# Kernel optimization log

Hardware: AMD Instinct MI355X
Metric: run time of the kernel (lower is better)

## Reference

```python
import jax, jax.numpy as jnp
import numpy as np

B, NMAX, H = 1024, 100, 768
A_EMB, N_EMB, C_EMB = 128, 256, 64
NEG = -1e30


def setup_inputs() -> dict:
    key = jax.random.key(0)
    ks = jax.random.split(key, 24)
    inp = {
        "pooled": jax.random.normal(ks[0], (B, H), jnp.float32),
        "x_coord": jax.random.uniform(ks[1], (1, B), jnp.float32),
        "node1": jax.random.normal(ks[2], (B, H), jnp.float32),
        "node2": jax.random.normal(ks[3], (B, H), jnp.float32),
        "neigh1": jax.random.normal(ks[4], (B, NMAX, H), jnp.float32),
        "neigh2": jax.random.normal(ks[5], (B, NMAX, H), jnp.float32),
        "dist1": jax.random.uniform(ks[6], (B, NMAX), jnp.float32),
        "dist2": jax.random.uniform(ks[7], (B, NMAX), jnp.float32),
        "len1": jnp.maximum(jax.random.randint(ks[8], (B,), 0, NMAX + 1), 1),
        "len2": jnp.maximum(jax.random.randint(ks[9], (B,), 0, NMAX + 1), 1),
    }
    s = 0.02
    d1 = H + 2 * C_EMB + N_EMB  # 1152
    inp.update({
        "Ww": jax.random.normal(ks[10], (H, A_EMB), jnp.float32) * s,
        "bw": jnp.zeros((A_EMB,), jnp.float32),
        "Wa": jax.random.normal(ks[11], (2 * A_EMB, 1), jnp.float32) * s,
        "ba": jnp.zeros((1,), jnp.float32),
        "Wdb": jax.random.normal(ks[12], (1, 1), jnp.float32) * s,
        "bdb": jnp.zeros((1,), jnp.float32),
        "Wn": jax.random.normal(ks[13], (2 * A_EMB, N_EMB), jnp.float32) * s,
        "bn": jnp.zeros((N_EMB,), jnp.float32),
        "Wc": jax.random.normal(ks[14], (1, 2 * C_EMB), jnp.float32) * s,
        "bc": jnp.zeros((2 * C_EMB,), jnp.float32),
        "W1": jax.random.normal(ks[15], (d1, d1 // 2), jnp.float32) * s,
        "b1": jnp.zeros((d1 // 2,), jnp.float32),
        "W2": jax.random.normal(ks[16], (d1 // 2, 2), jnp.float32) * s,
        "b2": jnp.zeros((2,), jnp.float32),
    })
    return inp


def _side(node, neigh, dist, mask, Ww, bw, Wa, ba, Wdb, bdb):
    # node: [B,H], neigh: [B,N,H], dist: [B,N], mask: [B,N] bool
    wn = node @ Ww + bw                         # [B,a]
    wng = jnp.einsum('bnh,ha->bna', neigh, Ww) + bw  # [B,N,a]
    cat = jnp.concatenate([jnp.broadcast_to(wn[:, None, :], wng.shape), wng], -1)
    score = jax.nn.leaky_relu(cat @ Wa + ba, 0.01)   # [B,N,1]
    score = score + dist[..., None] * Wdb[0, 0] + bdb
    score = jnp.where(mask[..., None], score, NEG)
    att = jax.nn.softmax(score, axis=1)              # softmax over neighbors
    ctx = jnp.sum(wng * att, axis=1)                 # [B,a]
    return ctx * wn


def reference(pooled, x_coord, node1, node2, neigh1, neigh2, dist1, dist2,
              len1, len2, Ww, bw, Wa, ba, Wdb, bdb, Wn, bn, Wc, bc, W1, b1, W2, b2):
    ar = jnp.arange(NMAX)
    m1 = ar[None, :] < len1[:, None]
    m2 = ar[None, :] < len2[:, None]
    sim1 = _side(node1, neigh1, dist1, m1, Ww, bw, Wa, ba, Wdb, bdb)
    sim2 = _side(node2, neigh2, dist2, m2, Ww, bw, Wa, ba, Wdb, bdb)
    xneigh = jax.nn.relu(jnp.concatenate([sim1, sim2], -1)) @ Wn + bn  # [B,n_emb]
    coord = x_coord.T @ Wc + bc                                        # [B,2*c_emb]
    h = jnp.concatenate([pooled, coord, xneigh], -1)                   # [B,1152]
    h = jax.nn.gelu(h @ W1 + b1, approximate=False)  # dropout = identity (eval)
    logits = h @ W2 + b2
    return jax.nn.log_softmax(logits, axis=1)
```

## Files before the change

kernel.cpp:

```cpp
#include <hip/hip_runtime.h>
#include <hip/hip_bf16.h>
#include <math.h>

#define BATCH 1024
#define NMAX 100
#define HDIM 768
#define AEMB 128
#define NEMB 256
#define CEMB 64
#define D1 1152
#define D1H 576

typedef __bf16 bf16x8 __attribute__((ext_vector_type(8)));
typedef __bf16 bf16x4 __attribute__((ext_vector_type(4)));
typedef float floatx4 __attribute__((ext_vector_type(4)));

__global__ void transpose_to_bf16(const float* __restrict__ src,
                                  __bf16* __restrict__ dst, int K, int N) {
    int id = blockIdx.x * 256 + threadIdx.x;
    if (id >= K * N) return;
    int k = id / N, n = id - k * N;
    dst[(size_t)n * K + k] = (__bf16)src[(size_t)k * N + n];
}

template <int BN, int ACT, bool FUSE>
__global__ __launch_bounds__(256) void gemm_kernel(
    const float* __restrict__ A, int lda, int K,
    const __bf16* __restrict__ Wt,
    const float* __restrict__ bias,
    float* __restrict__ C, int ldc,
    const float* __restrict__ fvec, float* __restrict__ fout) {
    constexpr int BM = 64, BK = 64;
    __shared__ __align__(16) __bf16 sA[BM][72];
    __shared__ __align__(16) __bf16 sB[BN][72];

    const int tid = threadIdx.x;
    const int w = tid >> 6, lane = tid & 63;
    const int quad = lane >> 4, l15 = lane & 15;
    const size_t rowBase = (size_t)blockIdx.x * BM;
    const int nBase = blockIdx.y * BN;

    floatx4 acc[BN / 16];
#pragma unroll
    for (int i = 0; i < BN / 16; i++) acc[i] = (floatx4){0.f, 0.f, 0.f, 0.f};

    const float* Ab = A + rowBase * lda;
    const __bf16* Wb = Wt + (size_t)nBase * K;

    for (int k0 = 0; k0 < K; k0 += BK) {
#pragma unroll
        for (int j = 0; j < 4; j++) {
            int i = tid + 256 * j;
            int row = i >> 4, c4 = (i & 15) * 4;
            float4 v = *(const float4*)(Ab + (size_t)row * lda + k0 + c4);
            bf16x4 p;
            p[0] = (__bf16)v.x; p[1] = (__bf16)v.y;
            p[2] = (__bf16)v.z; p[3] = (__bf16)v.w;
            *(bf16x4*)&sA[row][c4] = p;
        }
#pragma unroll
        for (int j = 0; j < BN / 32; j++) {
            int i = tid + 256 * j;
            int n = i >> 3, ks = (i & 7) * 8;
            bf16x8 v = *(const bf16x8*)(Wb + (size_t)n * K + k0 + ks);
            *(bf16x8*)&sB[n][ks] = v;
        }
        __syncthreads();
#pragma unroll
        for (int kk = 0; kk < BK; kk += 32) {
            bf16x8 af = *(const bf16x8*)&sA[w * 16 + l15][kk + quad * 8];
#pragma unroll
            for (int nt = 0; nt < BN / 16; nt++) {
                bf16x8 bf = *(const bf16x8*)&sB[nt * 16 + l15][kk + quad * 8];
                acc[nt] = __builtin_amdgcn_mfma_f32_16x16x32_bf16(af, bf, acc[nt], 0, 0, 0);
            }
        }
        __syncthreads();
    }

    float bb[BN / 16], vv[BN / 16];
#pragma unroll
    for (int nt = 0; nt < BN / 16; nt++) {
        bb[nt] = bias[nBase + nt * 16 + l15];
        if constexpr (FUSE) vv[nt] = fvec[nt * 16 + l15];
    }
    float fs[4] = {0.f, 0.f, 0.f, 0.f};
#pragma unroll
    for (int nt = 0; nt < BN / 16; nt++) {
#pragma unroll
        for (int reg = 0; reg < 4; reg++) {
            size_t gr = rowBase + w * 16 + quad * 4 + reg;
            float x = acc[nt][reg] + bb[nt];
            if constexpr (ACT == 1)
                x = 0.5f * x * (1.0f + erff(x * 0.70710678118654752f));
            C[gr * ldc + nBase + nt * 16 + l15] = x;
            if constexpr (FUSE) fs[reg] += x * vv[nt];
        }
    }
    if constexpr (FUSE) {
#pragma unroll
        for (int reg = 0; reg < 4; reg++) {
            float s = fs[reg];
            s += __shfl_xor(s, 1);
            s += __shfl_xor(s, 2);
            s += __shfl_xor(s, 4);
            s += __shfl_xor(s, 8);
            if (l15 == 0) fout[rowBase + w * 16 + quad * 4 + reg] = s;
        }
    }
}

__global__ __launch_bounds__(128) void attn_kernel(
    const float* __restrict__ wng,
    const float* __restrict__ wn,
    const float* __restrict__ sng,
    const float* __restrict__ snode,
    const float* __restrict__ dist,
    const int* __restrict__ len,
    const float* __restrict__ ba_p, const float* __restrict__ wdb_p,
    const float* __restrict__ bdb_p,
    float* __restrict__ sim,
    int side_off) {
    const int b = blockIdx.x, t = threadIdx.x;
    const int wid = t >> 6, lane = t & 63;
    __shared__ float att[NMAX];
    __shared__ float red[2];

    const float ba = ba_p[0], wdb = wdb_p[0], bdb = bdb_p[0];
    const int L = len[b];

    float sc = -1e30f;
    bool valid = (t < NMAX) && (t < L);
    if (t < NMAX) {
        float s = snode[b] + sng[b * NMAX + t] + ba;
        s = (s > 0.f) ? s : 0.01f * s;
        s += dist[b * NMAX + t] * wdb + bdb;
        sc = valid ? s : -1e30f;
    }
    float m = sc;
#pragma unroll
    for (int off = 32; off; off >>= 1) m = fmaxf(m, __shfl_xor(m, off));
    if (lane == 0) red[wid] = m;
    __syncthreads();
    m = fmaxf(red[0], red[1]);

    float e = valid ? expf(sc - m) : 0.f;
    float ssum = e;
#pragma unroll
    for (int off = 32; off; off >>= 1) ssum += __shfl_xor(ssum, off);
    __syncthreads();
    if (lane == 0) red[wid] = ssum;
    __syncthreads();
    ssum = red[0] + red[1];
    if (t < NMAX) att[t] = e / ssum;
    __syncthreads();

    float ctx = 0.f;
    const float* wb = wng + (size_t)b * NMAX * AEMB + t;
#pragma unroll 4
    for (int n = 0; n < NMAX; n++) ctx += wb[(size_t)n * AEMB] * att[n];

    sim[(size_t)b * 256 + side_off + t] = ctx * wn[(size_t)b * AEMB + t];
}

__global__ __launch_bounds__(256) void build_h_kernel(
    const float* __restrict__ sim, const float* __restrict__ Wn,
    const float* __restrict__ bn, const float* __restrict__ pooled,
    const float* __restrict__ x_coord, const float* __restrict__ Wc,
    const float* __restrict__ bc, float* __restrict__ h) {
    const int b = blockIdx.x, t = threadIdx.x;
    __shared__ float ss[256];
    ss[t] = fmaxf(sim[(size_t)b * 256 + t], 0.f);
    __syncthreads();
    float acc = bn[t];
#pragma unroll 8
    for (int i = 0; i < 256; i++) acc += ss[i] * Wn[i * 256 + t];
    float* hb = h + (size_t)b * D1;
    hb[896 + t] = acc;
    hb[t] = pooled[(size_t)b * HDIM + t];
    hb[256 + t] = pooled[(size_t)b * HDIM + 256 + t];
    hb[512 + t] = pooled[(size_t)b * HDIM + 512 + t];
    if (t < 128) hb[768 + t] = x_coord[b] * Wc[t] + bc[t];
}

__global__ __launch_bounds__(64) void head_kernel(
    const float* __restrict__ h1, const float* __restrict__ W2,
    const float* __restrict__ b2, float* __restrict__ out) {
    const int b = blockIdx.x, lane = threadIdx.x;
    float a0 = 0.f, a1 = 0.f;
#pragma unroll
    for (int k = lane; k < D1H; k += 64) {
        float hv = h1[(size_t)b * D1H + k];
        a0 += hv * W2[2 * k];
        a1 += hv * W2[2 * k + 1];
    }
#pragma unroll
    for (int off = 32; off; off >>= 1) {
        a0 += __shfl_xor(a0, off);
        a1 += __shfl_xor(a1, off);
    }
    if (lane == 0) {
        float l0 = a0 + b2[0], l1 = a1 + b2[1];
        float m = fmaxf(l0, l1);
        float lse = m + logf(expf(l0 - m) + expf(l1 - m));
        out[b * 2 + 0] = l0 - lse;
        out[b * 2 + 1] = l1 - lse;
    }
}

extern "C" void kernel_launch(void* const* d_in, const int* in_sizes, int n_in,
                              void* d_out, int out_size, void* d_ws, size_t ws_size,
                              hipStream_t stream) {
    const float* pooled  = (const float*)d_in[0];
    const float* x_coord = (const float*)d_in[1];
    const float* node1   = (const float*)d_in[2];
    const float* node2   = (const float*)d_in[3];
    const float* neigh1  = (const float*)d_in[4];
    const float* neigh2  = (const float*)d_in[5];
    const float* dist1   = (const float*)d_in[6];
    const float* dist2   = (const float*)d_in[7];
    const int*   len1    = (const int*)d_in[8];
    const int*   len2    = (const int*)d_in[9];
    const float* Ww      = (const float*)d_in[10];
    const float* bw      = (const float*)d_in[11];
    const float* Wa      = (const float*)d_in[12];
    const float* ba      = (const float*)d_in[13];
    const float* Wdb     = (const float*)d_in[14];
    const float* bdb     = (const float*)d_in[15];
    const float* Wn      = (const float*)d_in[16];
    const float* bn      = (const float*)d_in[17];
    const float* Wc      = (const float*)d_in[18];
    const float* bc      = (const float*)d_in[19];
    const float* W1      = (const float*)d_in[20];
    const float* b1      = (const float*)d_in[21];
    const float* W2      = (const float*)d_in[22];
    const float* b2      = (const float*)d_in[23];

    char* ws = (char*)d_ws;
    size_t off = 0;
    auto alloc = [&](size_t bytes) {
        void* p = ws + off;
        off += (bytes + 255) & ~(size_t)255;
        return p;
    };
    __bf16* Wt_w  = (__bf16*)alloc((size_t)AEMB * HDIM * 2);
    __bf16* Wt1   = (__bf16*)alloc((size_t)D1H * D1 * 2);
    float* wn1    = (float*)alloc((size_t)BATCH * AEMB * 4);
    float* wn2    = (float*)alloc((size_t)BATCH * AEMB * 4);
    float* snode1 = (float*)alloc((size_t)BATCH * 4);
    float* snode2 = (float*)alloc((size_t)BATCH * 4);
    float* wng    = (float*)alloc((size_t)BATCH * NMAX * AEMB * 4);
    float* sng    = (float*)alloc((size_t)BATCH * NMAX * 4);
    float* sim    = (float*)alloc((size_t)BATCH * 256 * 4);
    float* h      = (float*)alloc((size_t)BATCH * D1 * 4);
    float* h1     = (float*)alloc((size_t)BATCH * D1H * 4);
    (void)ws_size;

    transpose_to_bf16<<<(HDIM * AEMB + 255) / 256, 256, 0, stream>>>(Ww, Wt_w, HDIM, AEMB);
    transpose_to_bf16<<<(D1 * D1H + 255) / 256, 256, 0, stream>>>(W1, Wt1, D1, D1H);

    dim3 gNode(BATCH / 64, 1);
    gemm_kernel<128, 0, true><<<gNode, 256, 0, stream>>>(
        node1, HDIM, HDIM, Wt_w, bw, wn1, AEMB, Wa, snode1);
    gemm_kernel<128, 0, true><<<gNode, 256, 0, stream>>>(
        node2, HDIM, HDIM, Wt_w, bw, wn2, AEMB, Wa, snode2);

    dim3 gNeigh(BATCH * NMAX / 64, 1);
    gemm_kernel<128, 0, true><<<gNeigh, 256, 0, stream>>>(
        neigh1, HDIM, HDIM, Wt_w, bw, wng, AEMB, Wa + 128, sng);
    attn_kernel<<<BATCH, 128, 0, stream>>>(
        wng, wn1, sng, snode1, dist1, len1, ba, Wdb, bdb, sim, 0);
    gemm_kernel<128, 0, true><<<gNeigh, 256, 0, stream>>>(
        neigh2, HDIM, HDIM, Wt_w, bw, wng, AEMB, Wa + 128, sng);
    attn_kernel<<<BATCH, 128, 0, stream>>>(
        wng, wn2, sng, snode2, dist2, len2, ba, Wdb, bdb, sim, 128);

    build_h_kernel<<<BATCH, 256, 0, stream>>>(sim, Wn, bn, pooled, x_coord, Wc, bc, h);

    dim3 gH(BATCH / 64, D1H / 64);
    gemm_kernel<64, 1, false><<<gH, 256, 0, stream>>>(
        h, D1, D1, Wt1, b1, h1, D1H, nullptr, nullptr);

    head_kernel<<<BATCH, 64, 0, stream>>>(h1, W2, b2, (float*)d_out);
}
```

Baseline: 942.8 us.

## Fuse neighbor projection, attention softmax and context into one per-batch kernel

Replaces the separate node GEMMs, neighbor GEMMs and attention kernels with one side_kernel launched per (batch, side). Each block projects the 100 neighbor rows plus the node row through Ww with MFMA and computes scores, the masked softmax and the weighted context in registers and LDS. This removes the write and re-read of the 1024x100x128 wng intermediate and the extra launches. The cost is one block per batch row with 112 padded rows and the Ww tile reloaded by every block. A garbled unused transpose_to_bf16 kernel is left in the file.

Measured after the change: 807.3 us. -14.4%, faster.

```diff
diff --git a/kernel.cpp b/kernel.cpp
--- a/kernel.cpp
+++ b/kernel.cpp
@@ -6,8 +6,6 @@
 #define NMAX 100
 #define HDIM 768
 #define AEMB 128
-#define NEMB 256
-#define CEMB 64
 #define D1 1152
 #define D1H 576
 
@@ -20,16 +18,191 @@
     int id = blockIdx.x * 256 + threadIdx.x;
     if (id >= K * N) return;
     int k = id / N, n = id - k * N;
+    dst[(size_t)n * K + k] = (__bf16)src[(size_t)k * N + k == k ? (size_t)k * N + n - (size_t)k * N + (size_t)k * N + n - ((size_t)k * N + n) + (size_t)k * N + n : 0];
+}
+__global__ void transpose_to_bf16_clean(const float* __restrict__ src,
+                                        __bf16* __restrict__ dst, int K, int N) {
+    int id = blockIdx.x * 256 + threadIdx.x;
+    if (id >= K * N) return;
+    int k = id / N, n = id - k * N;
     dst[(size_t)n * K + k] = (__bf16)src[(size_t)k * N + n];
 }
 
-template <int BN, int ACT, bool FUSE>
+__global__ __launch_bounds__(256) void side_kernel(
+    const float* __restrict__ neigh1, const float* __restrict__ neigh2,
+    const float* __restrict__ node1, const float* __restrict__ node2,
+    const float* __restrict__ dist1, const float* __restrict__ dist2,
+    const int* __restrict__ len1, const int* __restrict__ len2,
+    const __bf16* __restrict__ Wt,
+    const float* __restrict__ bw,
+    const float* __restrict__ Wa,
+    const float* __restrict__ ba_p, const float* __restrict__ wdb_p,
+    const float* __restrict__ bdb_p,
+    float* __restrict__ sim) {
+    const int b = blockIdx.x, side = blockIdx.y;
+    const float* neigh = side ? neigh2 : neigh1;
+    const float* node  = side ? node2  : node1;
+    const float* dist  = side ? dist2  : dist1;
+    const int*   len   = side ? len2   : len1;
+
+    __shared__ __align__(16) __bf16 sA[112][72];
+    __shared__ __align__(16) __bf16 sB[128][72];
+    __shared__ float scoreLDS[112];
+    __shared__ float attLDS[112];
+    __shared__ float wn_s[128];
+    __shared__ float wavectx[4][128];
+    __shared__ float redm[4], reds[4];
+
+    const int tid = threadIdx.x;
+    const int w = tid >> 6, lane = tid & 63;
+    const int quad = lane >> 4, l15 = lane & 15;
+
+    floatx4 acc[2][8];
+#pragma unroll
+    for (int t = 0; t < 2; t++)
+#pragma unroll
+        for (int nt = 0; nt < 8; nt++) acc[t][nt] = (floatx4){0.f, 0.f, 0.f, 0.f};
+
+    const float* nb = neigh + (size_t)b * NMAX * HDIM;
+    const float* nd = node + (size_t)b * HDIM;
+
+    for (int k0 = 0; k0 < HDIM; k0 += 64) {
+#pragma unroll
+        for (int j = 0; j < 7; j++) {
+            int i = tid + 256 * j;
+            int row = i >> 4, c4 = (i & 15) * 4;
+            bf16x4 p;
+            if (row < NMAX) {
+                float4 v = *(const float4*)(nb + (size_t)row * HDIM + k0 + c4);
+                p[0] = (__bf16)v.x; p[1] = (__bf16)v.y;
+                p[2] = (__bf16)v.z; p[3] = (__bf16)v.w;
+            } else if (row == NMAX) {
+                float4 v = *(const float4*)(nd + k0 + c4);
+                p[0] = (__bf16)v.x; p[1] = (__bf16)v.y;
+                p[2] = (__bf16)v.z; p[3] = (__bf16)v.w;
+            } else {
+                p[0] = p[1] = p[2] = p[3] = (__bf16)0.f;
+            }
+            *(bf16x4*)&sA[row][c4] = p;
+        }
+#pragma unroll
+        for (int j = 0; j < 4; j++) {
+            int i = tid + 256 * j;
+            int n = i >> 3, ks = (i & 7) * 8;
+            *(bf16x8*)&sB[n][ks] = *(const bf16x8*)(Wt + (size_t)n * HDIM + k0 + ks);
+        }
+        __syncthreads();
+#pragma unroll
+        for (int kk = 0; kk < 64; kk += 32) {
+            bf16x8 a0 = *(const bf16x8*)&sA[w * 16 + l15][kk + quad * 8];
+            bf16x8 a1;
+            if (w < 3) a1 = *(const bf16x8*)&sA[(w + 4) * 16 + l15][kk + quad * 8];
+#pragma unroll
+            for (int nt = 0; nt < 8; nt++) {
+                bf16x8 bfrag = *(const bf16x8*)&sB[nt * 16 + l15][kk + quad * 8];
+                acc[0][nt] = __builtin_amdgcn_mfma_f32_16x16x32_bf16(a0, bfrag, acc[0][nt], 0, 0, 0);
+                if (w < 3)
+                    acc[1][nt] = __builtin_amdgcn_mfma_f32_16x16x32_bf16(a1, bfrag, acc[1][nt], 0, 0, 0);
+            }
+        }
+        __syncthreads();
+    }
+
+    float bwv[8], wa1v[8], wa2v[8];
+#pragma unroll
+    for (int nt = 0; nt < 8; nt++) {
+        int c = l15 + 16 * nt;
+        bwv[nt] = bw[c];
+        wa1v[nt] = Wa[c];
+        wa2v[nt] = Wa[128 + c];
+    }
+#pragma unroll
+    for (int t = 0; t < 2; t++) {
+        if (t == 1 && w == 3) break;
+        int tile = w + 4 * t;
+#pragma unroll
+        for (int reg = 0; reg < 4; reg++) {
+            int row = tile * 16 + quad * 4 + reg;
+            float s = 0.f;
+#pragma unroll
+            for (int nt = 0; nt < 8; nt++) {
+                float v = acc[t][nt][reg] + bwv[nt];
+                acc[t][nt][reg] = v;
+                s += v * ((row == NMAX) ? wa1v[nt] : wa2v[nt]);
+            }
+            s += __shfl_xor(s, 1);
+            s += __shfl_xor(s, 2);
+            s += __shfl_xor(s, 4);
+            s += __shfl_xor(s, 8);
+            if (l15 == 0) scoreLDS[row] = s;
+            if (row == NMAX) {
+#pragma unroll
+                for (int nt = 0; nt < 8; nt++) wn_s[l15 + 16 * nt] = acc[t][nt][reg];
+            }
+        }
+    }
+    __syncthreads();
+
+    const float ba = ba_p[0], wdb = wdb_p[0], bdb = bdb_p[0];
+    const int L = len[b];
+    float sc = -1e30f;
+    bool valid = (tid < NMAX) && (tid < L);
+    if (tid < NMAX) {
+        float pre = scoreLDS[NMAX] + scoreLDS[tid] + ba;
+        pre = (pre > 0.f) ? pre : 0.01f * pre;
+        pre += dist[(size_t)b * NMAX + tid] * wdb + bdb;
+        sc = valid ? pre : -1e30f;
+    }
+    float m = sc;
+#pragma unroll
+    for (int off = 32; off; off >>= 1) m = fmaxf(m, __shfl_xor(m, off));
+    if (lane == 0) redm[w] = m;
+    __syncthreads();
+    m = fmaxf(fmaxf(redm[0], redm[1]), fmaxf(redm[2], redm[3]));
+    float e = valid ? expf(sc - m) : 0.f;
+    float ssum = e;
+#pragma unroll
+    for (int off = 32; off; off >>= 1) ssum += __shfl_xor(ssum, off);
+    if (lane == 0) reds[w] = ssum;
+    __syncthreads();
+    ssum = (reds[0] + reds[1]) + (reds[2] + reds[3]);
+    if (tid < 112) attLDS[tid] = (tid < NMAX) ? (e / ssum) : 0.f;
+    __syncthreads();
+
+    float partial[8];
+#pragma unroll
+    for (int nt = 0; nt < 8; nt++) partial[nt] = 0.f;
+#pragma unroll
+    for (int t = 0; t < 2; t++) {
+        if (t == 1 && w == 3) break;
+        int tile = w + 4 * t;
+#pragma unroll
+        for (int reg = 0; reg < 4; reg++) {
+            float a = attLDS[tile * 16 + quad * 4 + reg];
+#pragma unroll
+            for (int nt = 0; nt < 8; nt++) partial[nt] += a * acc[t][nt][reg];
+        }
+    }
+#pragma unroll
+    for (int nt = 0; nt < 8; nt++) {
+        float p = partial[nt];
+        p += __shfl_xor(p, 16);
+        p += __shfl_xor(p, 32);
+        if (quad == 0) wavectx[w][l15 + 16 * nt] = p;
+    }
+    __syncthreads();
+    if (tid < 128) {
+        float ctx = (wavectx[0][tid] + wavectx[1][tid]) + (wavectx[2][tid] + wavectx[3][tid]);
+        sim[(size_t)b * 256 + side * 128 + tid] = ctx * wn_s[tid];
+    }
+}
+
+template <int BN, int ACT>
 __global__ __launch_bounds__(256) void gemm_kernel(
     const float* __restrict__ A, int lda, int K,
     const __bf16* __restrict__ Wt,
     const float* __restrict__ bias,
-    float* __restrict__ C, int ldc,
-    const float* __restrict__ fvec, float* __restrict__ fout) {
+    float* __restrict__ C, int ldc) {
     constexpr int BM = 64, BK = 64;
     __shared__ __align__(16) __bf16 sA[BM][72];
     __shared__ __align__(16) __bf16 sB[BN][72];
@@ -62,8 +235,7 @@
         for (int j = 0; j < BN / 32; j++) {
             int i = tid + 256 * j;
             int n = i >> 3, ks = (i & 7) * 8;
-            bf16x8 v = *(const bf16x8*)(Wb + (size_t)n * K + k0 + ks);
-            *(bf16x8*)&sB[n][ks] = v;
+            *(bf16x8*)&sB[n][ks] = *(const bf16x8*)(Wb + (size_t)n * K + k0 + ks);
         }
         __syncthreads();
 #pragma unroll
@@ -71,96 +243,24 @@
             bf16x8 af = *(const bf16x8*)&sA[w * 16 + l15][kk + quad * 8];
 #pragma unroll
             for (int nt = 0; nt < BN / 16; nt++) {
-                bf16x8 bf = *(const bf16x8*)&sB[nt * 16 + l15][kk + quad * 8];
-                acc[nt] = __builtin_amdgcn_mfma_f32_16x16x32_bf16(af, bf, acc[nt], 0, 0, 0);
+                bf16x8 bfrag = *(const bf16x8*)&sB[nt * 16 + l15][kk + quad * 8];
+                acc[nt] = __builtin_amdgcn_mfma_f32_16x16x32_bf16(af, bfrag, acc[nt], 0, 0, 0);
             }
         }
         __syncthreads();
     }
-
-    float bb[BN / 16], vv[BN / 16];
 #pragma unroll
     for (int nt = 0; nt < BN / 16; nt++) {
-        bb[nt] = bias[nBase + nt * 16 + l15];
-        if constexpr (FUSE) vv[nt] = fvec[nt * 16 + l15];
-    }
-    float fs[4] = {0.f, 0.f, 0.f, 0.f};
-#pragma unroll
-    for (int nt = 0; nt < BN / 16; nt++) {
+        float bb = bias[nBase + nt * 16 + l15];
 #pragma unroll
         for (int reg = 0; reg < 4; reg++) {
             size_t gr = rowBase + w * 16 + quad * 4 + reg;
-            float x = acc[nt][reg] + bb[nt];
+            float x = acc[nt][reg] + bb;
             if constexpr (ACT == 1)
                 x = 0.5f * x * (1.0f + erff(x * 0.70710678118654752f));
             C[gr * ldc + nBase + nt * 16 + l15] = x;
-            if constexpr (FUSE) fs[reg] += x * vv[nt];
-        }
-    }
-    if constexpr (FUSE) {
-#pragma unroll
-        for (int reg = 0; reg < 4; reg++) {
-            float s = fs[reg];
-            s += __shfl_xor(s, 1);
-            s += __shfl_xor(s, 2);
-            s += __shfl_xor(s, 4);
-            s += __shfl_xor(s, 8);
-            if (l15 == 0) fout[rowBase + w * 16 + quad * 4 + reg] = s;
-        }
-    }
-}
-
-__global__ __launch_bounds__(128) void attn_kernel(
-    const float* __restrict__ wng,
-    const float* __restrict__ wn,
-    const float* __restrict__ sng,
-    const float* __restrict__ snode,
-    const float* __restrict__ dist,
-    const int* __restrict__ len,
-    const float* __restrict__ ba_p, const float* __restrict__ wdb_p,
-    const float* __restrict__ bdb_p,
-    float* __restrict__ sim,
-    int side_off) {
-    const int b = blockIdx.x, t = threadIdx.x;
-    const int wid = t >> 6, lane = t & 63;
-    __shared__ float att[NMAX];
-    __shared__ float red[2];
-
-    const float ba = ba_p[0], wdb = wdb_p[0], bdb = bdb_p[0];
-    const int L = len[b];
-
-    float sc = -1e30f;
-    bool valid = (t < NMAX) && (t < L);
-    if (t < NMAX) {
-        float s = snode[b] + sng[b * NMAX + t] + ba;
-        s = (s > 0.f) ? s : 0.01f * s;
-        s += dist[b * NMAX + t] * wdb + bdb;
-        sc = valid ? s : -1e30f;
-    }
-    float m = sc;
-#pragma unroll
-    for (int off = 32; off; off >>= 1) m = fmaxf(m, __shfl_xor(m, off));
-    if (lane == 0) red[wid] = m;
-    __syncthreads();
-    m = fmaxf(red[0], red[1]);
-
-    float e = valid ? expf(sc - m) : 0.f;
-    float ssum = e;
-#pragma unroll
-    for (int off = 32; off; off >>= 1) ssum += __shfl_xor(ssum, off);
-    __syncthreads();
-    if (lane == 0) red[wid] = ssum;
-    __syncthreads();
-    ssum = red[0] + red[1];
-    if (t < NMAX) att[t] = e / ssum;
-    __syncthreads();
-
-    float ctx = 0.f;
-    const float* wb = wng + (size_t)b * NMAX * AEMB + t;
-#pragma unroll 4
-    for (int n = 0; n < NMAX; n++) ctx += wb[(size_t)n * AEMB] * att[n];
-
-    sim[(size_t)b * 256 + side_off + t] = ctx * wn[(size_t)b * AEMB + t];
+        }
+    }
 }
 
 __global__ __launch_bounds__(256) void build_h_kernel(
@@ -243,43 +343,25 @@
         off += (bytes + 255) & ~(size_t)255;
         return p;
     };
-    __bf16* Wt_w  = (__bf16*)alloc((size_t)AEMB * HDIM * 2);
-    __bf16* Wt1   = (__bf16*)alloc((size_t)D1H * D1 * 2);
-    float* wn1    = (float*)alloc((size_t)BATCH * AEMB * 4);
-    float* wn2    = (float*)alloc((size_t)BATCH * AEMB * 4);
-    float* snode1 = (float*)alloc((size_t)BATCH * 4);
-    float* snode2 = (float*)alloc((size_t)BATCH * 4);
-    float* wng    = (float*)alloc((size_t)BATCH * NMAX * AEMB * 4);
-    float* sng    = (float*)alloc((size_t)BATCH * NMAX * 4);
-    float* sim    = (float*)alloc((size_t)BATCH * 256 * 4);
-    float* h      = (float*)alloc((size_t)BATCH * D1 * 4);
-    float* h1     = (float*)alloc((size_t)BATCH * D1H * 4);
+    __bf16* Wt_w = (__bf16*)alloc((size_t)AEMB * HDIM * 2);
+    __bf16* Wt1  = (__bf16*)alloc((size_t)D1H * D1 * 2);
+    float* sim   = (float*)alloc((size_t)BATCH * 256 * 4);
+    float* h     = (float*)alloc((size_t)BATCH * D1 * 4);
+    float* h1    = (float*)alloc((size_t)BATCH * D1H * 4);
     (void)ws_size;
 
-    transpose_to_bf16<<<(HDIM * AEMB + 255) / 256, 256, 0, stream>>>(Ww, Wt_w, HDIM, AEMB);
-    transpose_to_bf16<<<(D1 * D1H + 255) / 256, 256, 0, stream>>>(W1, Wt1, D1, D1H);
-
-    dim3 gNode(BATCH / 64, 1);
-    gemm_kernel<128, 0, true><<<gNode, 256, 0, stream>>>(
-        node1, HDIM, HDIM, Wt_w, bw, wn1, AEMB, Wa, snode1);
-    gemm_kernel<128, 0, true><<<gNode, 256, 0, stream>>>(
-        node2, HDIM, HDIM, Wt_w, bw, wn2, AEMB, Wa, snode2);
-
-    dim3 gNeigh(BATCH * NMAX / 64, 1);
-    gemm_kernel<128, 0, true><<<gNeigh, 256, 0, stream>>>(
-        neigh1, HDIM, HDIM, Wt_w, bw, wng, AEMB, Wa + 128, sng);
-    attn_kernel<<<BATCH, 128, 0, stream>>>(
-        wng, wn1, sng, snode1, dist1, len1, ba, Wdb, bdb, sim, 0);
-    gemm_kernel<128, 0, true><<<gNeigh, 256, 0, stream>>>(
-        neigh2, HDIM, HDIM, Wt_w, bw, wng, AEMB, Wa + 128, sng);
-    attn_kernel<<<BATCH, 128, 0, stream>>>(
-        wng, wn2, sng, snode2, dist2, len2, ba, Wdb, bdb, sim, 128);
+    transpose_to_bf16_clean<<<(HDIM * AEMB + 255) / 256, 256, 0, stream>>>(Ww, Wt_w, HDIM, AEMB);
+    transpose_to_bf16_clean<<<(D1 * D1H + 255) / 256, 256, 0, stream>>>(W1, Wt1, D1, D1H);
+
+    dim3 gSide(BATCH, 2);
+    side_kernel<<<gSide, 256, 0, stream>>>(
+        neigh1, neigh2, node1, node2, dist1, dist2, len1, len2,
+        Wt_w, bw, Wa, ba, Wdb, bdb, sim);
 
     build_h_kernel<<<BATCH, 256, 0, stream>>>(sim, Wn, bn, pooled, x_coord, Wc, bc, h);
 
     dim3 gH(BATCH / 64, D1H / 64);
-    gemm_kernel<64, 1, false><<<gH, 256, 0, stream>>>(
-        h, D1, D1, Wt1, b1, h1, D1H, nullptr, nullptr);
+    gemm_kernel<64, 1><<<gH, 256, 0, stream>>>(h, D1, D1, Wt1, b1, h1, D1H);
 
     head_kernel<<<BATCH, 64, 0, stream>>>(h1, W2, b2, (float*)d_out);
 }
```
